# Kernel optimization log

Hardware: AMD Instinct MI355X
Metric: run time of the kernel (lower is better)

The kernel has to match this reference:

```python
import jax, jax.numpy as jnp
import numpy as np

NUM_HEADS = 12


def setup_inputs() -> dict:
    key = jax.random.key(0)
    ks = jax.random.split(key, 8)
    B, N, C = 1024, 196, 384
    hd = C // NUM_HEADS  # 32
    return {
        "x": jax.random.normal(ks[0], (B, N, C), jnp.float32),
        "qkv_w": jax.random.normal(ks[1], (3 * C, C), jnp.float32) * 0.02,
        "qkv_b": jax.random.normal(ks[2], (3 * C,), jnp.float32) * 0.02,
        "proj_w": jax.random.normal(ks[3], (C, C), jnp.float32) * 0.02,
        "proj_b": jax.random.normal(ks[4], (C,), jnp.float32) * 0.02,
        "dwc_w": jax.random.normal(ks[5], (hd, 1, 5, 5), jnp.float32) * 0.02,
        "dwc_b": jax.random.normal(ks[6], (hd,), jnp.float32) * 0.02,
        "pos_enc": jax.random.normal(ks[7], (1, N, C), jnp.float32) * 0.02,
    }


def reference(x, qkv_w, qkv_b, proj_w, proj_b, dwc_w, dwc_b, pos_enc):
    B, N, C = x.shape
    h = NUM_HEADS
    hd = C // h

    qkv = x @ qkv_w.T + qkv_b                      # [B, N, 3C]
    qkv = qkv.reshape(B, N, 3, C)
    q, k, v = qkv[:, :, 0], qkv[:, :, 1], qkv[:, :, 2]
    k = k + pos_enc[:, :N, :]
    q = jax.nn.relu(q)
    k = jax.nn.relu(k)

    def split_heads(t):  # [B, N, (h c)] -> [(B h), N, c]
        return t.reshape(B, N, h, hd).transpose(0, 2, 1, 3).reshape(B * h, N, hd)

    q, k, v = split_heads(q), split_heads(k), split_heads(v)
    i, j, c, d = q.shape[-2], k.shape[-2], k.shape[-1], v.shape[-1]

    z = 1.0 / (jnp.einsum('bic,bc->bi', q, k.sum(axis=1)) + 1e-6)  # [Bh, N]
    if i * j * (c + d) > c * d * (i + j):
        kv = jnp.einsum('bjc,bjd->bcd', k, v)                      # [Bh, c, d]
        out = jnp.einsum('bic,bcd,bi->bid', q, kv, z)
    else:
        qk = jnp.einsum('bic,bjc->bij', q, k)
        out = jnp.einsum('bij,bjd,bi->bid', qk, v, z)

    # depthwise conv residual on v: [(B h), N, c] -> NCHW window grid
    w = int(N ** 0.5)
    fm = v.reshape(B * h, w, w, hd).transpose(0, 3, 1, 2)          # [Bh, c, w, w]
    fm = jax.lax.conv_general_dilated(
        fm, dwc_w, window_strides=(1, 1), padding='SAME',
        feature_group_count=hd,
        dimension_numbers=('NCHW', 'OIHW', 'NCHW'))
    fm = fm + dwc_b[None, :, None, None]
    fm = fm.transpose(0, 2, 3, 1).reshape(B * h, N, hd)

    out = out + fm
    out = out.reshape(B, h, N, hd).transpose(0, 2, 1, 3).reshape(B, N, C)
    out = out @ proj_w.T + proj_b
    return out
```

## Files before the change

### kernel.cpp

```cpp
#include <hip/hip_runtime.h>
#include <hip/hip_fp16.h>
#include <cstdint>

#define DI __device__ __forceinline__

typedef __attribute__((ext_vector_type(8))) _Float16 hx8;
typedef __attribute__((ext_vector_type(4))) float f4;
typedef unsigned short u16;
typedef unsigned int u32;
typedef __attribute__((ext_vector_type(4))) u32 u32x4;

constexpr int NB = 1024;
constexpr int NN = 196;
constexpr int NC = 384;
constexpr int NH = 12;
constexpr int HD = 32;
constexpr int C3 = 3 * NC;
constexpr int PH = NN * HD;

constexpr size_t SZ_TH   = (size_t)NB * NH * PH * 2;
constexpr size_t OFF_Q   = 0;
constexpr size_t OFF_K   = SZ_TH;
constexpr size_t OFF_V   = 2 * SZ_TH;
constexpr size_t OFF_WQF = 3 * SZ_TH;
constexpr size_t SZ_WQ   = (size_t)C3 * NC * 2;
constexpr size_t OFF_WPF = OFF_WQF + SZ_WQ;
constexpr size_t SZ_WP   = (size_t)NC * NC * 2;
constexpr size_t OFF_XF  = OFF_WPF + SZ_WP;

DI void gload_lds16(const void* g, void* l) {
  using GP = const void __attribute__((address_space(1)))*;
  using LP = void __attribute__((address_space(3)))*;
  __builtin_amdgcn_global_load_lds((GP)g, (LP)l, 16, 0, 0);
}

DI u32 cvt_pk_bf16(float lo, float hi) {
  u32 r;
  asm volatile("v_cvt_pk_bf16_f32 %0, %1, %2" : "=v"(r) : "v"(lo), "v"(hi));
  return r;
}
DI float bflo(u32 p) { return __uint_as_float(p << 16); }
DI float bfhi(u32 p) { return __uint_as_float(p & 0xffff0000u); }
DI float h2f(u16 v)  { _Float16 h = __builtin_bit_cast(_Float16, v); return (float)h; }
DI u16   f2h(float f){ _Float16 h = (_Float16)f; return __builtin_bit_cast(u16, h); }

__global__ void split_weights(const float* __restrict__ qw, const float* __restrict__ pw,
                              u16* __restrict__ qf, u16* __restrict__ pf)
{
  int i = blockIdx.x * 256 + threadIdx.x;
  if (i < C3 * NC) qf[i] = f2h(qw[i]);
  if (i < NC * NC) pf[i] = f2h(pw[i]);
}

__global__ void cvt_x_f16(const float* __restrict__ x, u16* __restrict__ xf)
{
  size_t i = ((size_t)blockIdx.x * 256 + threadIdx.x) * 8;
  f4 a = *(const f4*)(x + i);
  f4 b = *(const f4*)(x + i + 4);
  u16 o[8];
  o[0]=f2h(a[0]); o[1]=f2h(a[1]); o[2]=f2h(a[2]); o[3]=f2h(a[3]);
  o[4]=f2h(b[0]); o[5]=f2h(b[1]); o[6]=f2h(b[2]); o[7]=f2h(b[3]);
  u32x4 pk;
#pragma unroll
  for (int j = 0; j < 4; ++j) pk[j] = (u32)o[2*j] | ((u32)o[2*j+1] << 16);
  *(u32x4*)(xf + i) = pk;
}

__global__ __launch_bounds__(256, 4) void qkv_gemm_f16(
    const u16* __restrict__ xf, const u16* __restrict__ wf,
    const float* __restrict__ bias, const float* __restrict__ pos,
    u16* __restrict__ qo, u16* __restrict__ ko, u16* __restrict__ vo)
{
  __shared__ __align__(16) char lds[2][16384];
  const int tid  = threadIdx.x;
  const int lane = tid & 63, wv = tid >> 6;
  const int L  = ((int)blockIdx.x & 7) * 1764 + ((int)blockIdx.x >> 3);
  const int rt = L / 9, ct = L - rt * 9;
  const int m0 = rt * 128, t0 = ct * 128;

  const u16* spA[2];
  const u16* spB[2];
#pragma unroll
  for (int j = 0; j < 2; ++j) {
    int g = j * 256 + tid;
    int row = g >> 2, slot = g & 3;
    int c = slot ^ (row & 3);
    spA[j] = xf + (size_t)(m0 + row) * NC + c * 8;
    spB[j] = wf + (size_t)(t0 + row) * NC + c * 8;
  }

  auto stage = [&](char* buf) {
#pragma unroll
    for (int j = 0; j < 2; ++j) {
      gload_lds16(spA[j], buf + (j * 256 + tid) * 16);
      spA[j] += 32;
      gload_lds16(spB[j], buf + 8192 + (j * 256 + tid) * 16);
      spB[j] += 32;
    }
  };

  const int wm = (wv & 1) * 64, wn = (wv >> 1) * 64;
  const int l15 = lane & 15, l4 = lane >> 4;
  const int sl = l4 ^ (l15 & 3);
  int aoff[4], boff[4];
#pragma unroll
  for (int i = 0; i < 4; ++i) {
    aoff[i] = (wm + i * 16 + l15) * 64 + sl * 16;
    boff[i] = 8192 + (wn + i * 16 + l15) * 64 + sl * 16;
  }

  f4 acc[4][4];
  const f4 fz = {0.f, 0.f, 0.f, 0.f};
#pragma unroll
  for (int i = 0; i < 4; ++i)
#pragma unroll
    for (int j = 0; j < 4; ++j) acc[i][j] = fz;

  stage(lds[0]);
  for (int kt = 0; kt < 12; ++kt) {
    __syncthreads();
    if (kt < 11) stage(lds[(kt + 1) & 1]);
    char* buf = lds[kt & 1];
    hx8 af[4], bf4[4];
#pragma unroll
    for (int i = 0; i < 4; ++i) {
      af[i]  = *(const hx8*)(buf + aoff[i]);
      bf4[i] = *(const hx8*)(buf + boff[i]);
    }
#pragma unroll
    for (int mi = 0; mi < 4; ++mi)
#pragma unroll
      for (int ni = 0; ni < 4; ++ni)
        acc[mi][ni] = __builtin_amdgcn_mfma_f32_16x16x32_f16(af[mi], bf4[ni], acc[mi][ni], 0, 0, 0);
  }

  const int s = ct / 3, cb = (ct - s * 3) * 128;
  float biasv[4];
#pragma unroll
  for (int ni = 0; ni < 4; ++ni) biasv[ni] = bias[t0 + wn + ni * 16 + l15];
#pragma unroll
  for (int mi = 0; mi < 4; ++mi) {
#pragma unroll
    for (int rr = 0; rr < 4; ++rr) {
      int m = m0 + wm + mi * 16 + l4 * 4 + rr;
      int b = m / 196, n = m - b * 196;
      size_t rowb = (size_t)b * 75264 + (size_t)n * 32;
#pragma unroll
      for (int ni = 0; ni < 4; ++ni) {
        int c = cb + wn + ni * 16 + l15;
        float val = acc[mi][ni][rr] + biasv[ni];
        size_t idx = rowb + (size_t)(c >> 5) * 6272 + (c & 31);
        if (s == 0)      { qo[idx] = f2h(fmaxf(val, 0.f)); }
        else if (s == 1) { ko[idx] = f2h(fmaxf(val + pos[n * 384 + c], 0.f)); }
        else             { vo[idx] = (u16)cvt_pk_bf16(val, val); }
      }
    }
  }
}

__global__ __launch_bounds__(256, 4) void attn_conv(
    const u16* __restrict__ q, const u16* k,
    const u16* __restrict__ v16, u16* y,
    const float* __restrict__ dwc_w, const float* __restrict__ dwc_b)
{
  __shared__ __align__(16) u16  sv[NN * 40];
  __shared__ __align__(16) u16  sfm[NN * 40];
  __shared__ __align__(16) float skv[32 * 36];
  __shared__ float sksum[32];

  const int tid = threadIdx.x;
  const size_t base = (size_t)blockIdx.x * PH;
  const u16* vp = v16 + base;
  const u16* kp = k + base;
  const u16* qp = q + base;
  u16* yp = y + base;
  char* svb  = (char*)sv;
  char* sfmb = (char*)sfm;

  for (int c = tid; c < 784; c += 256) {
    u32x4 pk = *(const u32x4*)(vp + c * 8);
    *(u32x4*)(svb + (c >> 2) * 80 + (c & 3) * 16) = pk;
  }
  __syncthreads();

  {
    const int c = tid >> 3, ns = tid & 7;
    float acc[33];
#pragma unroll
    for (int d = 0; d < 33; ++d) acc[d] = 0.f;
    for (int i = 0; i < 25; ++i) {
      int n = i * 8 + ns;
      if (n < 196) {
        float kc = h2f(kp[n * 32 + c]);
#pragma unroll
        for (int g = 0; g < 4; ++g) {
          u32x4 r = *(const u32x4*)(svb + n * 80 + g * 16);
#pragma unroll
          for (int j = 0; j < 4; ++j) {
            acc[g * 8 + 2 * j]     += kc * bflo(r[j]);
            acc[g * 8 + 2 * j + 1] += kc * bfhi(r[j]);
          }
        }
        acc[32] += kc;
      }
    }
#pragma unroll
    for (int off = 1; off <= 4; off <<= 1) {
#pragma unroll
      for (int d = 0; d < 33; ++d) acc[d] += __shfl_xor(acc[d], off);
    }
    if (ns == 0) {
#pragma unroll
      for (int d4 = 0; d4 < 32; d4 += 4) {
        f4 w; w[0] = acc[d4]; w[1] = acc[d4+1]; w[2] = acc[d4+2]; w[3] = acc[d4+3];
        *(f4*)&skv[c * 36 + d4] = w;
      }
      sksum[c] = acc[32];
    }
  }

  {
    const int dp = tid & 15, py = tid >> 4;
    if (py < 14) {
      const int d0 = 2 * dp;
      float fm0[14], fm1[14];
      const float b0 = dwc_b[d0], b1 = dwc_b[d0 + 1];
#pragma unroll
      for (int px = 0; px < 14; ++px) { fm0[px] = b0; fm1[px] = b1; }
#pragma unroll
      for (int ky = 0; ky < 5; ++ky) {
        int yy = py + ky - 2;
        if (yy < 0 || yy >= 14) continue;
        float w0[5], w1[5];
#pragma unroll
        for (int t = 0; t < 5; ++t) {
          w0[t] = dwc_w[d0 * 25 + ky * 5 + t];
          w1[t] = dwc_w[(d0 + 1) * 25 + ky * 5 + t];
        }
        float r0[14], r1[14];
#pragma unroll
        for (int xx = 0; xx < 14; ++xx) {
          u32 pr = *(const u32*)(svb + (yy * 14 + xx) * 80 + dp * 4);
          r0[xx] = bflo(pr); r1[xx] = bfhi(pr);
        }
#pragma unroll
        for (int px = 0; px < 14; ++px) {
#pragma unroll
          for (int kx = 0; kx < 5; ++kx) {
            int xx = px + kx - 2;
            if (xx < 0 || xx > 13) continue;
            fm0[px] += w0[kx] * r0[xx];
            fm1[px] += w1[kx] * r1[xx];
          }
        }
      }
#pragma unroll
      for (int px = 0; px < 14; ++px)
        *(u32*)(sfmb + (py * 14 + px) * 80 + dp * 4) = cvt_pk_bf16(fm0[px], fm1[px]);
    }
  }
  __syncthreads();

  {
    const int dp = tid & 15, ng = tid >> 4;
    const int d0 = 2 * dp;
    float kv0[32], kv1[32], ks[32];
#pragma unroll
    for (int c = 0; c < 32; ++c) {
      const float* p = &skv[c * 36 + d0];
      kv0[c] = p[0]; kv1[c] = p[1];
    }
#pragma unroll
    for (int c = 0; c < 32; ++c) ks[c] = sksum[c];
#pragma unroll 2
    for (int i = 0; i < 13; ++i) {
      int n = i * 16 + ng;
      if (n < 196) {
        float o0 = 0.f, o1 = 0.f, pz = 0.f;
#pragma unroll
        for (int g = 0; g < 4; ++g) {
          u32x4 qw = *(const u32x4*)(qp + (size_t)n * 32 + g * 8);
#pragma unroll
          for (int j = 0; j < 4; ++j) {
            float q0 = h2f((u16)(qw[j] & 0xffffu));
            float q1 = h2f((u16)(qw[j] >> 16));
            int c = g * 8 + 2 * j;
            o0 += q0 * kv0[c] + q1 * kv0[c + 1];
            o1 += q0 * kv1[c] + q1 * kv1[c + 1];
            pz += q0 * ks[c]  + q1 * ks[c + 1];
          }
        }
        float z = 1.f / (pz + 1e-6f);
        u32 fmp = *(const u32*)(sfmb + n * 80 + dp * 4);
        float r0 = fmaf(o0, z, bflo(fmp));
        float r1 = fmaf(o1, z, bfhi(fmp));
        *(u32*)(yp + n * 32 + d0) = (u32)f2h(r0) | ((u32)f2h(r1) << 16);
      }
    }
  }
}

__global__ __launch_bounds__(256, 4) void proj_gemm_f16(
    const u16* __restrict__ yf, const u16* __restrict__ wf,
    const float* __restrict__ bias, float* __restrict__ out)
{
  __shared__ __align__(16) char lds[2][16384];
  const int tid  = threadIdx.x;
  const int lane = tid & 63, wv = tid >> 6;
  const int L  = ((int)blockIdx.x & 7) * 588 + ((int)blockIdx.x >> 3);
  const int rt = L / 3, ct = L - rt * 3;
  const int m0 = rt * 128, t0 = ct * 128;

  const u16* spA[2];
  const u16* spB[2];
#pragma unroll
  for (int j = 0; j < 2; ++j) {
    int g = j * 256 + tid;
    int row = g >> 2, slot = g & 3;
    int c = slot ^ (row & 3);
    int m = m0 + row;
    int b = m / 196, n = m - b * 196;
    spA[j] = yf + (size_t)b * 75264 + n * 32 + c * 8;
    spB[j] = wf + (size_t)(t0 + row) * NC + c * 8;
  }

  auto stage = [&](char* buf) {
#pragma unroll
    for (int j = 0; j < 2; ++j) {
      gload_lds16(spA[j], buf + (j * 256 + tid) * 16);
      spA[j] += 6272;
      gload_lds16(spB[j], buf + 8192 + (j * 256 + tid) * 16);
      spB[j] += 32;
    }
  };

  const int wm = (wv & 1) * 64, wn = (wv >> 1) * 64;
  const int l15 = lane & 15, l4 = lane >> 4;
  const int sl = l4 ^ (l15 & 3);
  int aoff[4], boff[4];
#pragma unroll
  for (int i = 0; i < 4; ++i) {
    aoff[i] = (wm + i * 16 + l15) * 64 + sl * 16;
    boff[i] = 8192 + (wn + i * 16 + l15) * 64 + sl * 16;
  }

  f4 acc[4][4];
  const f4 fz = {0.f, 0.f, 0.f, 0.f};
#pragma unroll
  for (int i = 0; i < 4; ++i)
#pragma unroll
    for (int j = 0; j < 4; ++j) acc[i][j] = fz;

  stage(lds[0]);
  for (int kt = 0; kt < 12; ++kt) {
    __syncthreads();
    if (kt < 11) stage(lds[(kt + 1) & 1]);
    char* buf = lds[kt & 1];
    hx8 af[4], bf4[4];
#pragma unroll
    for (int i = 0; i < 4; ++i) {
      af[i]  = *(const hx8*)(buf + aoff[i]);
      bf4[i] = *(const hx8*)(buf + boff[i]);
    }
#pragma unroll
    for (int mi = 0; mi < 4; ++mi)
#pragma unroll
      for (int ni = 0; ni < 4; ++ni)
        acc[mi][ni] = __builtin_amdgcn_mfma_f32_16x16x32_f16(af[mi], bf4[ni], acc[mi][ni], 0, 0, 0);
  }

  float biasv[4];
#pragma unroll
  for (int ni = 0; ni < 4; ++ni) biasv[ni] = bias[t0 + wn + ni * 16 + l15];
#pragma unroll
  for (int mi = 0; mi < 4; ++mi) {
#pragma unroll
    for (int rr = 0; rr < 4; ++rr) {
      int m = m0 + wm + mi * 16 + l4 * 4 + rr;
      size_t ob = (size_t)m * 384 + t0 + wn;
#pragma unroll
      for (int ni = 0; ni < 4; ++ni)
        out[ob + ni * 16 + l15] = acc[mi][ni][rr] + biasv[ni];
    }
  }
}

extern "C" void kernel_launch(void* const* d_in, const int* in_sizes, int n_in,
                              void* d_out, int out_size, void* d_ws, size_t ws_size,
                              hipStream_t stream)
{
  const float* x      = (const float*)d_in[0];
  const float* qkv_w  = (const float*)d_in[1];
  const float* qkv_b  = (const float*)d_in[2];
  const float* proj_w = (const float*)d_in[3];
  const float* proj_b = (const float*)d_in[4];
  const float* dwc_w  = (const float*)d_in[5];
  const float* dwc_b  = (const float*)d_in[6];
  const float* pos    = (const float*)d_in[7];
  float* out = (float*)d_out;
  char* ws = (char*)d_ws;

  u16* qb  = (u16*)(ws + OFF_Q);
  u16* kb  = (u16*)(ws + OFF_K);
  u16* vb  = (u16*)(ws + OFF_V);
  u16* wqf = (u16*)(ws + OFF_WQF);
  u16* wpf = (u16*)(ws + OFF_WPF);
  u16* xf  = (u16*)(ws + OFF_XF);
  u16* yb  = (u16*)(ws + OFF_K);

  split_weights<<<1728, 256, 0, stream>>>(qkv_w, proj_w, wqf, wpf);
  cvt_x_f16<<<37632, 256, 0, stream>>>(x, xf);
  qkv_gemm_f16<<<14112, 256, 0, stream>>>(xf, wqf, qkv_b, pos, qb, kb, vb);
  attn_conv<<<12288, 256, 0, stream>>>(qb, kb, vb, yb, dwc_w, dwc_b);
  proj_gemm_f16<<<4704, 256, 0, stream>>>(yb, wpf, proj_b, out);
}
```

Before: 1.064 ms.

## Store K/V transposed and padded, compute attention kv and output with MFMA

The QKV GEMM epilogue now writes K and V per head in a transposed [channel][token] layout padded to 208 tokens, with the pad zeroed in split_weights. V is kept in fp16 instead of bf16. The attention kernel loads K^T and V^T into LDS with direct global-to-LDS loads and computes K^T·V and Q·KV with 32x32x16 f16 MFMA instead of scalar FMA loops. The depthwise conv is re-partitioned to one channel-row per thread reading from the transposed V. This targets the scalar-ALU-bound attention stage, at the cost of scattered 2-byte transposed stores in the GEMM epilogue and fp16 rounding of kv.

```diff
diff --git a/kernel.cpp b/kernel.cpp
--- a/kernel.cpp
+++ b/kernel.cpp
@@ -5,9 +5,11 @@
 #define DI __device__ __forceinline__
 
 typedef __attribute__((ext_vector_type(8))) _Float16 hx8;
+typedef __attribute__((ext_vector_type(16))) float f32x16;
 typedef __attribute__((ext_vector_type(4))) float f4;
 typedef unsigned short u16;
 typedef unsigned int u32;
+typedef unsigned long long u64;
 typedef __attribute__((ext_vector_type(4))) u32 u32x4;
 
 constexpr int NB = 1024;
@@ -17,12 +19,16 @@
 constexpr int HD = 32;
 constexpr int C3 = 3 * NC;
 constexpr int PH = NN * HD;
-
-constexpr size_t SZ_TH   = (size_t)NB * NH * PH * 2;
+constexpr int KP = 208;
+constexpr int HP = 32 * KP;
+constexpr int NHEADS = NB * NH;
+
+constexpr size_t SZ_Q    = (size_t)NHEADS * PH * 2;
+constexpr size_t SZ_TP   = (size_t)NHEADS * HP * 2;
 constexpr size_t OFF_Q   = 0;
-constexpr size_t OFF_K   = SZ_TH;
-constexpr size_t OFF_V   = 2 * SZ_TH;
-constexpr size_t OFF_WQF = 3 * SZ_TH;
+constexpr size_t OFF_K   = SZ_Q;
+constexpr size_t OFF_V   = OFF_K + SZ_TP;
+constexpr size_t OFF_WQF = OFF_V + SZ_TP;
 constexpr size_t SZ_WQ   = (size_t)C3 * NC * 2;
 constexpr size_t OFF_WPF = OFF_WQF + SZ_WQ;
 constexpr size_t SZ_WP   = (size_t)NC * NC * 2;
@@ -34,22 +40,21 @@
   __builtin_amdgcn_global_load_lds((GP)g, (LP)l, 16, 0, 0);
 }
 
-DI u32 cvt_pk_bf16(float lo, float hi) {
-  u32 r;
-  asm volatile("v_cvt_pk_bf16_f32 %0, %1, %2" : "=v"(r) : "v"(lo), "v"(hi));
-  return r;
-}
-DI float bflo(u32 p) { return __uint_as_float(p << 16); }
-DI float bfhi(u32 p) { return __uint_as_float(p & 0xffff0000u); }
 DI float h2f(u16 v)  { _Float16 h = __builtin_bit_cast(_Float16, v); return (float)h; }
 DI u16   f2h(float f){ _Float16 h = (_Float16)f; return __builtin_bit_cast(u16, h); }
 
 __global__ void split_weights(const float* __restrict__ qw, const float* __restrict__ pw,
-                              u16* __restrict__ qf, u16* __restrict__ pf)
+                              u16* __restrict__ qf, u16* __restrict__ pf,
+                              u16* ktg, u16* vtg)
 {
   int i = blockIdx.x * 256 + threadIdx.x;
   if (i < C3 * NC) qf[i] = f2h(qw[i]);
   if (i < NC * NC) pf[i] = f2h(pw[i]);
+  for (u32 t = (u32)i; t < 786432u; t += 442368u) {
+    u32 head = t >> 6; int r = t & 63;
+    u16* p = ((r & 32) ? vtg : ktg) + (size_t)head * HP + (size_t)(r & 31) * KP + 196;
+    *(u64*)(p) = 0; *(u64*)(p + 4) = 0; *(u64*)(p + 8) = 0;
+  }
 }
 
 __global__ void cvt_x_f16(const float* __restrict__ x, u16* __restrict__ xf)
@@ -144,157 +149,146 @@
     for (int rr = 0; rr < 4; ++rr) {
       int m = m0 + wm + mi * 16 + l4 * 4 + rr;
       int b = m / 196, n = m - b * 196;
-      size_t rowb = (size_t)b * 75264 + (size_t)n * 32;
 #pragma unroll
       for (int ni = 0; ni < 4; ++ni) {
         int c = cb + wn + ni * 16 + l15;
         float val = acc[mi][ni][rr] + biasv[ni];
-        size_t idx = rowb + (size_t)(c >> 5) * 6272 + (c & 31);
-        if (s == 0)      { qo[idx] = f2h(fmaxf(val, 0.f)); }
-        else if (s == 1) { ko[idx] = f2h(fmaxf(val + pos[n * 384 + c], 0.f)); }
-        else             { vo[idx] = (u16)cvt_pk_bf16(val, val); }
-      }
-    }
-  }
-}
-
-__global__ __launch_bounds__(256, 4) void attn_conv(
-    const u16* __restrict__ q, const u16* k,
-    const u16* __restrict__ v16, u16* y,
-    const float* __restrict__ dwc_w, const float* __restrict__ dwc_b)
-{
-  __shared__ __align__(16) u16  sv[NN * 40];
-  __shared__ __align__(16) u16  sfm[NN * 40];
-  __shared__ __align__(16) float skv[32 * 36];
-  __shared__ float sksum[32];
-
-  const int tid = threadIdx.x;
-  const size_t base = (size_t)blockIdx.x * PH;
-  const u16* vp = v16 + base;
-  const u16* kp = k + base;
-  const u16* qp = q + base;
-  u16* yp = y + base;
-  char* svb  = (char*)sv;
-  char* sfmb = (char*)sfm;
-
-  for (int c = tid; c < 784; c += 256) {
-    u32x4 pk = *(const u32x4*)(vp + c * 8);
-    *(u32x4*)(svb + (c >> 2) * 80 + (c & 3) * 16) = pk;
-  }
-  __syncthreads();
-
-  {
-    const int c = tid >> 3, ns = tid & 7;
-    float acc[33];
-#pragma unroll
-    for (int d = 0; d < 33; ++d) acc[d] = 0.f;
-    for (int i = 0; i < 25; ++i) {
-      int n = i * 8 + ns;
-      if (n < 196) {
-        float kc = h2f(kp[n * 32 + c]);
-#pragma unroll
-        for (int g = 0; g < 4; ++g) {
-          u32x4 r = *(const u32x4*)(svb + n * 80 + g * 16);
-#pragma unroll
-          for (int j = 0; j < 4; ++j) {
-            acc[g * 8 + 2 * j]     += kc * bflo(r[j]);
-            acc[g * 8 + 2 * j + 1] += kc * bfhi(r[j]);
-          }
-        }
-        acc[32] += kc;
-      }
-    }
-#pragma unroll
-    for (int off = 1; off <= 4; off <<= 1) {
-#pragma unroll
-      for (int d = 0; d < 33; ++d) acc[d] += __shfl_xor(acc[d], off);
-    }
-    if (ns == 0) {
-#pragma unroll
-      for (int d4 = 0; d4 < 32; d4 += 4) {
-        f4 w; w[0] = acc[d4]; w[1] = acc[d4+1]; w[2] = acc[d4+2]; w[3] = acc[d4+3];
-        *(f4*)&skv[c * 36 + d4] = w;
-      }
-      sksum[c] = acc[32];
-    }
-  }
-
-  {
-    const int dp = tid & 15, py = tid >> 4;
-    if (py < 14) {
-      const int d0 = 2 * dp;
-      float fm0[14], fm1[14];
-      const float b0 = dwc_b[d0], b1 = dwc_b[d0 + 1];
-#pragma unroll
-      for (int px = 0; px < 14; ++px) { fm0[px] = b0; fm1[px] = b1; }
-#pragma unroll
-      for (int ky = 0; ky < 5; ++ky) {
-        int yy = py + ky - 2;
-        if (yy < 0 || yy >= 14) continue;
-        float w0[5], w1[5];
-#pragma unroll
-        for (int t = 0; t < 5; ++t) {
-          w0[t] = dwc_w[d0 * 25 + ky * 5 + t];
-          w1[t] = dwc_w[(d0 + 1) * 25 + ky * 5 + t];
-        }
-        float r0[14], r1[14];
-#pragma unroll
-        for (int xx = 0; xx < 14; ++xx) {
-          u32 pr = *(const u32*)(svb + (yy * 14 + xx) * 80 + dp * 4);
-          r0[xx] = bflo(pr); r1[xx] = bfhi(pr);
-        }
-#pragma unroll
-        for (int px = 0; px < 14; ++px) {
-#pragma unroll
-          for (int kx = 0; kx < 5; ++kx) {
-            int xx = px + kx - 2;
-            if (xx < 0 || xx > 13) continue;
-            fm0[px] += w0[kx] * r0[xx];
-            fm1[px] += w1[kx] * r1[xx];
-          }
+        int head = c >> 5, cc = c & 31;
+        if (s == 0) {
+          qo[((size_t)b * 12 + head) * PH + (size_t)n * 32 + cc] = f2h(fmaxf(val, 0.f));
+        } else {
+          size_t ti = ((size_t)b * 12 + head) * HP + (size_t)cc * KP + n;
+          if (s == 1) ko[ti] = f2h(fmaxf(val + pos[n * 384 + c], 0.f));
+          else        vo[ti] = f2h(val);
         }
       }
-#pragma unroll
-      for (int px = 0; px < 14; ++px)
-        *(u32*)(sfmb + (py * 14 + px) * 80 + dp * 4) = cvt_pk_bf16(fm0[px], fm1[px]);
-    }
-  }
+    }
+  }
+}
+
+__global__ __launch_bounds__(256, 4) void attn_conv(
+    const u16* __restrict__ q, const u16* kt, const u16* __restrict__ vt,
+    u16* y, const float* __restrict__ dwc_w, const float* __restrict__ dwc_b)
+{
+  __shared__ __align__(16) char smem[30096];
+  u16*   sKT = (u16*)smem;
+  u16*   sVT = (u16*)(smem + 13312);
+  u16*   sKV = (u16*)(smem + 26624);
+  float* sZ  = (float*)(smem + 29184);
+  float* sKS = (float*)(smem + 29968);
+
+  const int tid  = threadIdx.x;
+  const int lane = tid & 63, wv = tid >> 6;
+  const int r31 = lane & 31, hi = lane >> 5;
+  const size_t bh = blockIdx.x;
+  const u16* qh = q  + bh * PH;
+  const u16* kh = kt + bh * HP;
+  const u16* vh = vt + bh * HP;
+  u16*       yh = y  + bh * HP;
+
+  for (int i = tid; i < 832; i += 256) gload_lds16(kh + i * 8, smem + i * 16);
+  for (int i = tid; i < 832; i += 256) gload_lds16(vh + i * 8, smem + 13312 + i * 16);
   __syncthreads();
 
+  if (wv == 0) {
+    f32x16 kacc = {0,0,0,0,0,0,0,0,0,0,0,0,0,0,0,0};
+#pragma unroll
+    for (int kk = 0; kk < 13; ++kk) {
+      hx8 a = *(const hx8*)(sKT + r31 * KP + kk * 16 + hi * 8);
+      hx8 b = *(const hx8*)(sVT + r31 * KP + kk * 16 + hi * 8);
+      kacc = __builtin_amdgcn_mfma_f32_32x32x16_f16(a, b, kacc, 0, 0, 0);
+    }
+#pragma unroll
+    for (int r = 0; r < 16; ++r) {
+      int cc = (r & 3) + 8 * (r >> 2) + 4 * hi;
+      sKV[r31 * 40 + cc] = f2h(kacc[r]);
+    }
+  }
+
   {
-    const int dp = tid & 15, ng = tid >> 4;
-    const int d0 = 2 * dp;
-    float kv0[32], kv1[32], ks[32];
-#pragma unroll
-    for (int c = 0; c < 32; ++c) {
-      const float* p = &skv[c * 36 + d0];
-      kv0[c] = p[0]; kv1[c] = p[1];
-    }
-#pragma unroll
-    for (int c = 0; c < 32; ++c) ks[c] = sksum[c];
-#pragma unroll 2
-    for (int i = 0; i < 13; ++i) {
-      int n = i * 16 + ng;
+    int c = tid >> 3, ns = tid & 7;
+    float s = 0.f;
+#pragma unroll
+    for (int i = 0; i < 26; ++i) s += h2f(sKT[c * KP + ns * 26 + i]);
+#pragma unroll
+    for (int off = 1; off <= 4; off <<= 1) s += __shfl_xor(s, off);
+    if (ns == 0) sKS[c] = s;
+  }
+  __syncthreads();
+
+  if (tid < 196) {
+    float pz = 0.f;
+#pragma unroll
+    for (int g = 0; g < 4; ++g) {
+      u32x4 qw = *(const u32x4*)(qh + (size_t)tid * 32 + g * 8);
+#pragma unroll
+      for (int j = 0; j < 4; ++j) {
+        pz += h2f((u16)(qw[j] & 0xffffu)) * sKS[g * 8 + 2 * j]
+            + h2f((u16)(qw[j] >> 16))     * sKS[g * 8 + 2 * j + 1];
+      }
+    }
+    sZ[tid] = 1.f / (pz + 1e-6f);
+  }
+
+  u16* sFM = sKT;
+  auto conv_unit = [&](int u) {
+    int d = u & 31, py = u >> 5;
+    float fm[14];
+    float bv = dwc_b[d];
+#pragma unroll
+    for (int px = 0; px < 14; ++px) fm[px] = bv;
+#pragma unroll
+    for (int ky = 0; ky < 5; ++ky) {
+      int yy = py + ky - 2;
+      if (yy < 0 || yy >= 14) continue;
+      float w[5];
+#pragma unroll
+      for (int t = 0; t < 5; ++t) w[t] = dwc_w[d * 25 + ky * 5 + t];
+      float r[14];
+      const u32* vrow = (const u32*)(sVT + d * KP + yy * 14);
+#pragma unroll
+      for (int x2 = 0; x2 < 7; ++x2) {
+        u32 pr = vrow[x2];
+        r[2 * x2]     = h2f((u16)(pr & 0xffffu));
+        r[2 * x2 + 1] = h2f((u16)(pr >> 16));
+      }
+#pragma unroll
+      for (int px = 0; px < 14; ++px) {
+#pragma unroll
+        for (int kx = 0; kx < 5; ++kx) {
+          int xx = px + kx - 2;
+          if (xx < 0 || xx > 13) continue;
+          fm[px] += w[kx] * r[xx];
+        }
+      }
+    }
+#pragma unroll
+    for (int px = 0; px < 14; ++px)
+      sFM[d * KP + py * 14 + px] = f2h(fm[px]);
+  };
+  conv_unit(tid);
+  if (tid >= 64) conv_unit(tid + 192);
+  __syncthreads();
+
+#pragma unroll
+  for (int rep = 0; rep < 2; ++rep) {
+    int T = wv + rep * 4;
+    if (T >= 7) break;
+    const u16* qrow = qh + (size_t)(T * 32 + r31) * 32;
+    f32x16 acc = {0,0,0,0,0,0,0,0,0,0,0,0,0,0,0,0};
+#pragma unroll
+    for (int s = 0; s < 2; ++s) {
+      hx8 a = *(const hx8*)(qrow + hi * 8 + s * 16);
+      hx8 b = *(const hx8*)(sKV + r31 * 40 + hi * 8 + s * 16);
+      acc = __builtin_amdgcn_mfma_f32_32x32x16_f16(a, b, acc, 0, 0, 0);
+    }
+#pragma unroll
+    for (int r = 0; r < 16; ++r) {
+      int row = (r & 3) + 8 * (r >> 2) + 4 * hi;
+      int n = T * 32 + row;
       if (n < 196) {
-        float o0 = 0.f, o1 = 0.f, pz = 0.f;
-#pragma unroll
-        for (int g = 0; g < 4; ++g) {
-          u32x4 qw = *(const u32x4*)(qp + (size_t)n * 32 + g * 8);
-#pragma unroll
-          for (int j = 0; j < 4; ++j) {
-            float q0 = h2f((u16)(qw[j] & 0xffffu));
-            float q1 = h2f((u16)(qw[j] >> 16));
-            int c = g * 8 + 2 * j;
-            o0 += q0 * kv0[c] + q1 * kv0[c + 1];
-            o1 += q0 * kv1[c] + q1 * kv1[c + 1];
-            pz += q0 * ks[c]  + q1 * ks[c + 1];
-          }
-        }
-        float z = 1.f / (pz + 1e-6f);
-        u32 fmp = *(const u32*)(sfmb + n * 80 + dp * 4);
-        float r0 = fmaf(o0, z, bflo(fmp));
-        float r1 = fmaf(o1, z, bfhi(fmp));
-        *(u32*)(yp + n * 32 + d0) = (u32)f2h(r0) | ((u32)f2h(r1) << 16);
+        float val = acc[r] * sZ[n] + h2f(sFM[r31 * KP + n]);
+        yh[n * 32 + r31] = f2h(val);
       }
     }
   }
@@ -320,7 +314,7 @@
     int c = slot ^ (row & 3);
     int m = m0 + row;
     int b = m / 196, n = m - b * 196;
-    spA[j] = yf + (size_t)b * 75264 + n * 32 + c * 8;
+    spA[j] = yf + (size_t)b * (12 * HP) + (size_t)n * 32 + c * 8;
     spB[j] = wf + (size_t)(t0 + row) * NC + c * 8;
   }
 
@@ -328,7 +322,7 @@
 #pragma unroll
     for (int j = 0; j < 2; ++j) {
       gload_lds16(spA[j], buf + (j * 256 + tid) * 16);
-      spA[j] += 6272;
+      spA[j] += HP;
       gload_lds16(spB[j], buf + 8192 + (j * 256 + tid) * 16);
       spB[j] += 32;
     }
@@ -408,7 +402,7 @@
   u16* xf  = (u16*)(ws + OFF_XF);
   u16* yb  = (u16*)(ws + OFF_K);
 
-  split_weights<<<1728, 256, 0, stream>>>(qkv_w, proj_w, wqf, wpf);
+  split_weights<<<1728, 256, 0, stream>>>(qkv_w, proj_w, wqf, wpf, kb, vb);
   cvt_x_f16<<<37632, 256, 0, stream>>>(x, xf);
   qkv_gemm_f16<<<14112, 256, 0, stream>>>(xf, wqf, qkv_b, pos, qb, kb, vb);
   attn_conv<<<12288, 256, 0, stream>>>(qb, kb, vb, yb, dwc_w, dwc_b);
```

New measurement: 1.158 ms. +8.9%, slower.
